# Optimization experiments

Measured on AMD Instinct MI355X. Metric: run time of the kernel, lower is better.

Reference implementation:

```python
import jax, jax.numpy as jnp
import numpy as np

BLOCK_SIZE = 256

def setup_inputs() -> dict:
    key = jax.random.key(0)
    k1, k2, k3 = jax.random.split(key, 3)
    B, H, S, D = 2, 16, 2048, 128
    return {
        "query": jax.random.normal(k1, (B, H, S, D), dtype=jnp.float32),
        "key": jax.random.normal(k2, (B, H, S, D), dtype=jnp.float32),
        "value": jax.random.normal(k3, (B, H, S, D), dtype=jnp.float32),
    }

def reference(query, key, value):
    # Faithful translation of the (non-flash) blocked attention:
    # for each query block i and key block j, a FULL softmax is taken over
    # just that key block, and the per-block outputs are summed over j.
    B, H, S, D = query.shape
    bs = min(BLOCK_SIZE, S)
    nb = S // bs  # S chosen to be a multiple of block_size
    scale = D ** -0.5
    q = query.reshape(B, H, nb, bs, D)
    k = key.reshape(B, H, nb, bs, D)
    v = value.reshape(B, H, nb, bs, D)
    # scores: [B,H,nb_q,nb_k,bs_q,bs_k]
    scores = jnp.einsum('bhiqd,bhjkd->bhijqk', q, k) * scale
    # per key-block softmax (over last axis only, NOT global online softmax)
    w = jax.nn.softmax(scores, axis=-1)
    # weighted values, summed over key blocks j (matches output += block_output)
    out = jnp.einsum('bhijqk,bhjkd->bhiqd', w, v)
    return out.reshape(B, H, S, D)
```

## Files before the change

kernel.cpp:

```cpp
#include <hip/hip_runtime.h>
#include <stdint.h>

#define S_LEN 2048
#define D_DIM 128

typedef __attribute__((ext_vector_type(8)))  short bf16x8;
typedef __attribute__((ext_vector_type(4)))  short bf16x4;
typedef __attribute__((ext_vector_type(4)))  float f32x4;
typedef __attribute__((ext_vector_type(2)))  float f32x2;
typedef __attribute__((ext_vector_type(16))) float f32x16;

__device__ __forceinline__ short f2bf(float f) {
  union { float f; uint32_t u; } c; c.f = f;
  uint32_t u = c.u;
  u += 0x7fffu + ((u >> 16) & 1u);
  return (short)(u >> 16);
}
__device__ __forceinline__ uint32_t pk2bf(float a, float b) {
#if __has_builtin(__builtin_amdgcn_cvt_pk_bf16_f32)
  typedef __attribute__((ext_vector_type(2))) __bf16 bf2;
  union { bf2 v; uint32_t u; } cv;
  cv.v = __builtin_amdgcn_cvt_pk_bf16_f32(a, b);
  return cv.u;
#else
  return (uint32_t)(uint16_t)f2bf(a) | (((uint32_t)(uint16_t)f2bf(b)) << 16);
#endif
}
__device__ __forceinline__ bf16x8 mk8(uint32_t a, uint32_t b, uint32_t c, uint32_t d) {
  union { uint32_t u[4]; bf16x8 v; } x;
  x.u[0] = a; x.u[1] = b; x.u[2] = c; x.u[3] = d;
  return x.v;
}
__device__ __forceinline__ void gl_lds16(const short* g, short* l) {
  __builtin_amdgcn_global_load_lds((const __attribute__((address_space(1))) void*)g,
                                   (__attribute__((address_space(3))) void*)l, 16, 0, 0);
}

__global__ __launch_bounds__(256) void pre_kernel(
    const float* __restrict__ K, const float* __restrict__ V,
    short* __restrict__ Kb, short* __restrict__ Vt) {
  const int t = threadIdx.x;
  if (blockIdx.x >= 512) {
    int i0 = (blockIdx.x - 512) * 256 + t;
#pragma unroll
    for (int r = 0; r < 4; ++r) {
      int i = i0 + r * 524288;
      f32x4 v = ((const f32x4*)K)[i];
      *(uint2*)(Kb + (size_t)i * 4) = make_uint2(pk2bf(v[0], v[1]), pk2bf(v[2], v[3]));
    }
    return;
  }
  __shared__ __align__(16) uint32_t sU[128][64];
  const int vb = blockIdx.x;
  const int bh = vb >> 4;
  const int k0 = (vb & 15) * 128;
  const float* src = V + ((size_t)bh * S_LEN + k0) * D_DIM;
  {
    const int a = t & 31;
    const int E = 2 * (a & 15);
    const float* s0 = src + (size_t)(t >> 5) * 2 * D_DIM + a * 4;
#pragma unroll
    for (int p = 0; p < 8; ++p) {
      f32x4 vA = *(const f32x4*)(s0 + p * 16 * D_DIM);
      f32x4 vB = *(const f32x4*)(s0 + p * 16 * D_DIM + D_DIM);
      const int k2 = p * 8 + (t >> 5);
      const int col = k2 ^ E;
#pragma unroll
      for (int j = 0; j < 4; ++j)
        sU[4 * a + j][col] = pk2bf(vA[j], vB[j]);
    }
  }
  __syncthreads();
  {
    const int d = t >> 1;
    const int E = 2 * ((t >> 3) & 15);
    short* out = Vt + ((size_t)bh * D_DIM + d) * S_LEN + k0 + (t & 1) * 8;
#pragma unroll
    for (int g = 0; g < 8; ++g) {
      const int pb = g * 16 + (t & 1) * 8;
      const int kb1 = ((pb >> 4) << 4) + ((pb & 15) ? 4 : 0);
      const int k2a = kb1 >> 1;
      const int k2b = k2a + 4;
      uint2 lo = *(const uint2*)&sU[d][k2a ^ E];
      uint2 hi = *(const uint2*)&sU[d][k2b ^ E];
      uint4 o; o.x = lo.x; o.y = lo.y; o.z = hi.x; o.w = hi.y;
      *(uint4*)(out + g * 16) = o;
    }
  }
}

__global__ __launch_bounds__(256, 2) void attn_main(
    const short* __restrict__ Kb, const short* __restrict__ Vt,
    const float* __restrict__ Q, float* __restrict__ O) {
  __shared__ __align__(16) short ring[2][16384];
  __shared__ __align__(16) short sP[4096];
  __shared__ float sRed[128];
  __shared__ float sLinv[64];

  const int t = threadIdx.x;
  const int w = t >> 6;
  const int lane = t & 63;
  const int l31 = lane & 31;
  const int hi = lane >> 5;
  const int h = w & 1;
  const int qp = w >> 1;

  const int b = blockIdx.x;
  const int bh = (b & 7) * 4 + ((b >> 3) & 3);
  const int q0 = (b >> 5) * 64;

  const short* Kh = Kb + (size_t)bh * S_LEN * D_DIM;
  const short* Vh = Vt + (size_t)bh * D_DIM * S_LEN;

  const int kKey = t >> 4;
  const int kG   = (t & 15) ^ (kKey & 15);
  const int vD   = t >> 3;
  const int vG   = (t & 7) ^ (vD & 7);

  auto stageK = [&](int key0, int slot) {
    const short* src = Kh + (size_t)(key0 + kKey) * D_DIM + kG * 8;
    short* dst = &ring[slot][t * 8];
#pragma unroll
    for (int r = 0; r < 4; ++r) gl_lds16(src + r * 16 * D_DIM, dst + r * 2048);
  };
  auto stageV = [&](int key0, int slot) {
    const short* src = Vh + (size_t)vD * S_LEN + key0 + vG * 8;
    short* dst = &ring[slot][8192 + t * 8];
#pragma unroll
    for (int r = 0; r < 4; ++r) gl_lds16(src + (size_t)r * 32 * S_LEN, dst + r * 2048);
  };

  bf16x8 qf[8];
  {
    const float QSCALE = 0.12751743f;
    const float* Qg = Q + ((size_t)bh * S_LEN + q0 + qp * 32 + l31) * D_DIM;
#pragma unroll
    for (int ks = 0; ks < 8; ++ks) {
      f32x4 a = *(const f32x4*)(Qg + ks * 16 + hi * 8);
      f32x4 c = *(const f32x4*)(Qg + ks * 16 + hi * 8 + 4);
      qf[ks] = mk8(pk2bf(a[0] * QSCALE, a[1] * QSCALE), pk2bf(a[2] * QSCALE, a[3] * QSCALE),
                   pk2bf(c[0] * QSCALE, c[1] * QSCALE), pk2bf(c[2] * QSCALE, c[3] * QSCALE));
    }
  }

  int aK[8];
#pragma unroll
  for (int ks = 0; ks < 8; ++ks)
    aK[ks] = (h * 32 + l31) * 128 + (((2 * ks + hi) ^ (l31 & 15)) << 3);
  int aV[4];
#pragma unroll
  for (int u = 0; u < 4; ++u)
    aV[u] = (h * 64 + l31) * 64 + (((u * 2 + hi) ^ (l31 & 7)) << 3);

  f32x16 oa[2], oj[2];
#pragma unroll
  for (int d = 0; d < 2; ++d)
#pragma unroll
    for (int r = 0; r < 16; ++r) { oa[d][r] = 0.f; oj[d][r] = 0.f; }

  float ssum = 0.f;
  const int spOwn = ((qp * 2 + h) * 2) * 512 + lane * 8;

  stageK(0, 0); stageV(0, 0);

  for (int j = 0; j < 8; ++j) {
#pragma unroll
    for (int c = 0; c < 4; ++c) {
      const int G = j * 4 + c;
      const int slot = G & 1;
      __syncthreads();
      if (G + 1 < 32) { stageK((G + 1) * 64, slot ^ 1); stageV((G + 1) * 64, slot ^ 1); }

      if (c == 0 && j > 0) {
        f32x4 lv[4];
#pragma unroll
        for (int g = 0; g < 4; ++g) lv[g] = *(const f32x4*)&sLinv[qp * 32 + g * 8 + hi * 4];
#pragma unroll
        for (int d = 0; d < 2; ++d)
#pragma unroll
          for (int r = 0; r < 16; ++r) {
            oa[d][r] += oj[d][r] * lv[r >> 2][r & 3];
            oj[d][r] = 0.f;
          }
      }

      const short* pK = &ring[slot][0];
      f32x16 sc;
#pragma unroll
      for (int r = 0; r < 16; ++r) sc[r] = 0.f;
#pragma unroll
      for (int ks = 0; ks < 8; ++ks) {
        bf16x8 a = *(const bf16x8*)(pK + aK[ks]);
        sc = __builtin_amdgcn_mfma_f32_32x32x16_bf16(a, qf[ks], sc, 0, 0, 0);
      }
#pragma unroll
      for (int r = 0; r < 16; ++r) sc[r] = exp2f(sc[r]);
      float ps = 0.f;
#pragma unroll
      for (int r = 0; r < 16; ++r) ps += sc[r];
      ssum += ps;

      bf16x8 pf[2];
#pragma unroll
      for (int t2 = 0; t2 < 2; ++t2) {
        pf[t2] = mk8(pk2bf(sc[8 * t2 + 0], sc[8 * t2 + 1]), pk2bf(sc[8 * t2 + 2], sc[8 * t2 + 3]),
                     pk2bf(sc[8 * t2 + 4], sc[8 * t2 + 5]), pk2bf(sc[8 * t2 + 6], sc[8 * t2 + 7]));
        *(bf16x8*)(sP + spOwn + t2 * 512) = pf[t2];
      }
      if (c == 3) {
        ssum += __shfl_xor(ssum, 32);
        if (lane < 32) sRed[(qp * 32 + l31) * 2 + h] = ssum;
        ssum = 0.f;
      }
      __syncthreads();
      if (c == 3 && h == 0 && lane < 32) {
        f32x2 s2 = *(const f32x2*)&sRed[(qp * 32 + l31) * 2];
        sLinv[qp * 32 + l31] = __fdividef(1.0f, s2[0] + s2[1]);
      }

      const short* pV = &ring[slot][8192];
#pragma unroll
      for (int hw = 0; hw < 2; ++hw)
#pragma unroll
        for (int t2 = 0; t2 < 2; ++t2) {
          bf16x8 a = (hw == h) ? pf[t2]
                               : *(const bf16x8*)(sP + ((qp * 2 + hw) * 2 + t2) * 512 + lane * 8);
#pragma unroll
          for (int dt = 0; dt < 2; ++dt) {
            bf16x8 bv = *(const bf16x8*)(pV + aV[hw * 2 + t2] + dt * 2048);
            oj[dt] = __builtin_amdgcn_mfma_f32_32x32x16_bf16(a, bv, oj[dt], 0, 0, 0);
          }
        }
    }
  }

  __syncthreads();
  {
    f32x4 lv[4];
#pragma unroll
    for (int g = 0; g < 4; ++g) lv[g] = *(const f32x4*)&sLinv[qp * 32 + g * 8 + hi * 4];
    float* Og = O + ((size_t)bh * S_LEN + q0) * D_DIM;
#pragma unroll
    for (int d = 0; d < 2; ++d)
#pragma unroll
      for (int r = 0; r < 16; ++r) {
        float val = oa[d][r] + oj[d][r] * lv[r >> 2][r & 3];
        int row = qp * 32 + (r & 3) + 8 * (r >> 2) + 4 * hi;
        int col = h * 64 + d * 32 + l31;
        Og[row * D_DIM + col] = val;
      }
  }
}

extern "C" void kernel_launch(void* const* d_in, const int* in_sizes, int n_in,
                              void* d_out, int out_size, void* d_ws, size_t ws_size,
                              hipStream_t stream) {
  const float* Q = (const float*)d_in[0];
  const float* K = (const float*)d_in[1];
  const float* V = (const float*)d_in[2];
  float* Out = (float*)d_out;
  const size_t tElems = (size_t)32 * S_LEN * D_DIM;

  short* Kb  = (short*)d_ws;
  short* Vtb = Kb + tElems;

  pre_kernel<<<2560, 256, 0, stream>>>(K, V, Kb, Vtb);
  attn_main<<<1024, 256, 0, stream>>>(Kb, Vtb, Q, Out);
}
```

Baseline: 232.8 us.

## Split PV work by key half per wave, drop P exchange and mid-step barrier

Each wave now multiplies its own P fragment (its half of the 64 keys) against all 128 value dims, instead of exchanging P through shared memory to cover half the dims. This removes the sP buffer, its stores and loads, and the second __syncthreads per step. Each wave also computes the reciprocal row sums directly from sRed, so the sLinv buffer goes away. In exchange each wave holds twice as many accumulator registers (oa/oj of 4 tiles each), and the two half-sums are reduced through shared memory in the epilogue. The larger register footprint may hurt occupancy under launch_bounds(256,2).

After: 319.3 us. 1.37x slower.

```diff
diff --git a/kernel.cpp b/kernel.cpp
--- a/kernel.cpp
+++ b/kernel.cpp
@@ -93,9 +93,7 @@
     const short* __restrict__ Kb, const short* __restrict__ Vt,
     const float* __restrict__ Q, float* __restrict__ O) {
   __shared__ __align__(16) short ring[2][16384];
-  __shared__ __align__(16) short sP[4096];
   __shared__ float sRed[128];
-  __shared__ float sLinv[64];
 
   const int t = threadIdx.x;
   const int w = t >> 6;
@@ -147,19 +145,30 @@
 #pragma unroll
   for (int ks = 0; ks < 8; ++ks)
     aK[ks] = (h * 32 + l31) * 128 + (((2 * ks + hi) ^ (l31 & 15)) << 3);
-  int aV[4];
-#pragma unroll
-  for (int u = 0; u < 4; ++u)
-    aV[u] = (h * 64 + l31) * 64 + (((u * 2 + hi) ^ (l31 & 7)) << 3);
-
-  f32x16 oa[2], oj[2];
-#pragma unroll
-  for (int d = 0; d < 2; ++d)
+  int aV[2];
+#pragma unroll
+  for (int t2 = 0; t2 < 2; ++t2)
+    aV[t2] = l31 * 64 + ((((2 * h + t2) * 2 + hi) ^ (l31 & 7)) << 3);
+
+  f32x16 oa[4], oj[4];
+#pragma unroll
+  for (int d = 0; d < 4; ++d)
 #pragma unroll
     for (int r = 0; r < 16; ++r) { oa[d][r] = 0.f; oj[d][r] = 0.f; }
 
   float ssum = 0.f;
-  const int spOwn = ((qp * 2 + h) * 2) * 512 + lane * 8;
+
+  auto loadLv = [&](f32x4* lv) {
+#pragma unroll
+    for (int g = 0; g < 4; ++g) {
+      f32x4 p0 = *(const f32x4*)&sRed[(qp * 32 + g * 8 + 4 * hi) * 2];
+      f32x4 p1 = *(const f32x4*)&sRed[(qp * 32 + g * 8 + 4 * hi) * 2 + 4];
+      lv[g][0] = __fdividef(1.0f, p0[0] + p0[1]);
+      lv[g][1] = __fdividef(1.0f, p0[2] + p0[3]);
+      lv[g][2] = __fdividef(1.0f, p1[0] + p1[1]);
+      lv[g][3] = __fdividef(1.0f, p1[2] + p1[3]);
+    }
+  };
 
   stageK(0, 0); stageV(0, 0);
 
@@ -173,10 +182,9 @@
 
       if (c == 0 && j > 0) {
         f32x4 lv[4];
-#pragma unroll
-        for (int g = 0; g < 4; ++g) lv[g] = *(const f32x4*)&sLinv[qp * 32 + g * 8 + hi * 4];
-#pragma unroll
-        for (int d = 0; d < 2; ++d)
+        loadLv(lv);
+#pragma unroll
+        for (int d = 0; d < 4; ++d)
 #pragma unroll
           for (int r = 0; r < 16; ++r) {
             oa[d][r] += oj[d][r] * lv[r >> 2][r & 3];
@@ -195,60 +203,69 @@
       }
 #pragma unroll
       for (int r = 0; r < 16; ++r) sc[r] = exp2f(sc[r]);
-      float ps = 0.f;
-#pragma unroll
-      for (int r = 0; r < 16; ++r) ps += sc[r];
-      ssum += ps;
+      {
+        float a0 = sc[0] + sc[1], a1 = sc[2] + sc[3], a2 = sc[4] + sc[5], a3 = sc[6] + sc[7];
+        float a4 = sc[8] + sc[9], a5 = sc[10] + sc[11], a6 = sc[12] + sc[13], a7 = sc[14] + sc[15];
+        float b0 = a0 + a1, b1 = a2 + a3, b2 = a4 + a5, b3 = a6 + a7;
+        ssum += (b0 + b1) + (b2 + b3);
+      }
 
       bf16x8 pf[2];
 #pragma unroll
-      for (int t2 = 0; t2 < 2; ++t2) {
+      for (int t2 = 0; t2 < 2; ++t2)
         pf[t2] = mk8(pk2bf(sc[8 * t2 + 0], sc[8 * t2 + 1]), pk2bf(sc[8 * t2 + 2], sc[8 * t2 + 3]),
                      pk2bf(sc[8 * t2 + 4], sc[8 * t2 + 5]), pk2bf(sc[8 * t2 + 6], sc[8 * t2 + 7]));
-        *(bf16x8*)(sP + spOwn + t2 * 512) = pf[t2];
-      }
       if (c == 3) {
         ssum += __shfl_xor(ssum, 32);
         if (lane < 32) sRed[(qp * 32 + l31) * 2 + h] = ssum;
         ssum = 0.f;
       }
-      __syncthreads();
-      if (c == 3 && h == 0 && lane < 32) {
-        f32x2 s2 = *(const f32x2*)&sRed[(qp * 32 + l31) * 2];
-        sLinv[qp * 32 + l31] = __fdividef(1.0f, s2[0] + s2[1]);
-      }
 
       const short* pV = &ring[slot][8192];
 #pragma unroll
-      for (int hw = 0; hw < 2; ++hw)
-#pragma unroll
-        for (int t2 = 0; t2 < 2; ++t2) {
-          bf16x8 a = (hw == h) ? pf[t2]
-                               : *(const bf16x8*)(sP + ((qp * 2 + hw) * 2 + t2) * 512 + lane * 8);
-#pragma unroll
-          for (int dt = 0; dt < 2; ++dt) {
-            bf16x8 bv = *(const bf16x8*)(pV + aV[hw * 2 + t2] + dt * 2048);
-            oj[dt] = __builtin_amdgcn_mfma_f32_32x32x16_bf16(a, bv, oj[dt], 0, 0, 0);
-          }
+      for (int t2 = 0; t2 < 2; ++t2) {
+        bf16x8 a = pf[t2];
+#pragma unroll
+        for (int dt = 0; dt < 4; ++dt) {
+          bf16x8 bv = *(const bf16x8*)(pV + aV[t2] + dt * 2048);
+          oj[dt] = __builtin_amdgcn_mfma_f32_32x32x16_bf16(a, bv, oj[dt], 0, 0, 0);
         }
+      }
     }
   }
 
   __syncthreads();
   {
     f32x4 lv[4];
-#pragma unroll
-    for (int g = 0; g < 4; ++g) lv[g] = *(const f32x4*)&sLinv[qp * 32 + g * 8 + hi * 4];
+    loadLv(lv);
+#pragma unroll
+    for (int d = 0; d < 4; ++d)
+#pragma unroll
+      for (int r = 0; r < 16; ++r)
+        oa[d][r] += oj[d][r] * lv[r >> 2][r & 3];
+
+    float* ex = (float*)&ring[0][0];
+#pragma unroll
+    for (int dtl = 0; dtl < 2; ++dtl) {
+      const int dt = 2 * (1 - h) + dtl;
+      float* dst = ex + ((qp * 2 + h) * 2 + dtl) * 1024 + lane * 16;
+#pragma unroll
+      for (int r = 0; r < 16; ++r) dst[r] = oa[dt][r];
+    }
+    __syncthreads();
     float* Og = O + ((size_t)bh * S_LEN + q0) * D_DIM;
 #pragma unroll
-    for (int d = 0; d < 2; ++d)
+    for (int dtl = 0; dtl < 2; ++dtl) {
+      const int dt = 2 * h + dtl;
+      const float* srcf = ex + ((qp * 2 + (1 - h)) * 2 + dtl) * 1024 + lane * 16;
 #pragma unroll
       for (int r = 0; r < 16; ++r) {
-        float val = oa[d][r] + oj[d][r] * lv[r >> 2][r & 3];
+        float val = oa[dt][r] + srcf[r];
         int row = qp * 32 + (r & 3) + 8 * (r >> 2) + 4 * hi;
-        int col = h * 64 + d * 32 + l31;
+        int col = dt * 32 + l31;
         Og[row * D_DIM + col] = val;
       }
+    }
   }
 }
 
```
